# Performance work log

Hardware: AMD Instinct MI355X
Metric: run time of the kernel (lower is better)

Reference implementation:

```python
import jax, jax.numpy as jnp
import numpy as np

N = 4096
IN_DIM, HID, OUT_DIM = 512, 256, 64
PROP_STEP = 10
LAM_HAT = 0.9
SCAD_A = 3.7
EPS = 1e-8


def setup_inputs() -> dict:
    key = jax.random.key(0)
    kA, kF, k1, k2 = jax.random.split(key, 4)
    # sparse symmetric 0/1 adjacency, zero diagonal (add_loops adds I later)
    u = jax.random.uniform(kA, (N, N), dtype=jnp.float32)
    A = (u < 0.005).astype(jnp.float32)
    A = jnp.maximum(A, A.T)
    A = A * (1.0 - jnp.eye(N, dtype=jnp.float32))
    F = jax.random.normal(kF, (N, IN_DIM), dtype=jnp.float32)
    W1 = jax.random.normal(k1, (IN_DIM, HID), dtype=jnp.float32) / np.sqrt(IN_DIM)
    b1 = jnp.zeros((HID,), dtype=jnp.float32)
    W2 = jax.random.normal(k2, (HID, OUT_DIM), dtype=jnp.float32) / np.sqrt(HID)
    b2 = jnp.zeros((OUT_DIM,), dtype=jnp.float32)
    raw_gamma = jnp.zeros((PROP_STEP,), dtype=jnp.float32)
    return {"A": A, "F": F, "W1": W1, "b1": b1, "W2": W2, "b2": b2,
            "raw_gamma": raw_gamma}


def reference(A, F, W1, b1, W2, b2, raw_gamma):
    lam = 1.0 / LAM_HAT - 1.0
    a = SCAD_A
    # MLP (dropout inactive at inference)
    F0 = jax.nn.relu(F @ W1 + b1) @ W2 + b2            # [N, out_dim]
    eye = jnp.eye(A.shape[0], dtype=A.dtype)
    A = A + eye                                        # add_loops
    D = A.sum(-1)                                      # [N]
    D_sq = jnp.sqrt(D)[:, None]                        # [N, 1]
    A_tilde = A / D_sq / D_sq.T                        # sym_norm: D^-1/2 A D^-1/2
    gammas = jax.nn.sigmoid(raw_gamma) * 2.0           # per-layer gamma in (0, 2)

    def step(Fc, gamma_k):
        Fn = Fc / D_sq
        nrm = jnp.linalg.norm(Fn, axis=-1, keepdims=True)
        Fu = Fn / jnp.maximum(nrm, 1e-12)
        # cosine distance in [0, 2]; detached as in torch (.detach())
        y = jax.lax.stop_gradient(1.0 - Fu @ Fu.T)     # [N, N]
        lam_k = jnp.maximum(gamma_k / a, EPS)
        t = a * lam_k
        safe_y = jnp.where(y <= 0.0, 1.0, y)
        w_mid = (t - y) / ((a - 1.0) * safe_y)
        # SCAD weight: 1 for y<=lam_k, linear decay on [lam_k, a*lam_k], 0 beyond
        W = jnp.where(y <= lam_k, 1.0, jnp.where(y <= t, w_mid, 0.0))
        W = W * (1.0 - eye)
        W = jnp.where(jnp.isnan(W), 1.0, W)
        Q_hat = ((W * A).sum(-1) / D + lam)[:, None]   # [N, 1]
        F_new = (W * A_tilde) @ Fc / Q_hat + lam * F0 / Q_hat
        return F_new, None

    F_out, _ = jax.lax.scan(step, F0, gammas)
    return F_out
```

## Files before the change

kernel.cpp:

```cpp
#include <hip/hip_runtime.h>
#include <hip/hip_bf16.h>

#define N_NODES 4096
#define IN_DIM  512
#define HID_DIM 256
#define OUT_DIM 64
#define PROP_STEP 10
#define MAX_DEG 128
#define KSPLIT  4
#define LAM_CONST (1.0f/0.9f - 1.0f)
#define SCAD_A 3.7f

__device__ __forceinline__ ushort f2bf(float f) {
    unsigned u = __float_as_uint(f);
    unsigned r = (u + 0x7FFFu + ((u >> 16) & 1u)) >> 16;
    return (ushort)r;
}
__device__ __forceinline__ unsigned pack2(float lo, float hi) {
    return (unsigned)f2bf(lo) | ((unsigned)f2bf(hi) << 16);
}
__device__ __forceinline__ float bflo(unsigned u) { return __uint_as_float(u << 16); }
__device__ __forceinline__ float bfhi(unsigned u) { return __uint_as_float(u & 0xFFFF0000u); }

__device__ __forceinline__ float wave_reduce_add(float v) {
#pragma unroll
    for (int off = 32; off > 0; off >>= 1) v += __shfl_xor(v, off, 64);
    return v;
}

__global__ __launch_bounds__(256) void build_graph(
    const float* __restrict__ A, int* __restrict__ ell, int* __restrict__ deg,
    float* __restrict__ invD, float* __restrict__ invDsq)
{
    int i = blockIdx.x;
    int t = threadIdx.x;
    __shared__ int cnt;
    if (t == 0) cnt = 0;
    __syncthreads();
    const float4* row = (const float4*)(A + (size_t)i * N_NODES);
    for (int q = t; q < N_NODES / 4; q += 256) {
        float4 v = row[q];
        if (v.x != 0.0f) { int p = atomicAdd(&cnt, 1); if (p < MAX_DEG) ell[i * MAX_DEG + p] = q * 4 + 0; }
        if (v.y != 0.0f) { int p = atomicAdd(&cnt, 1); if (p < MAX_DEG) ell[i * MAX_DEG + p] = q * 4 + 1; }
        if (v.z != 0.0f) { int p = atomicAdd(&cnt, 1); if (p < MAX_DEG) ell[i * MAX_DEG + p] = q * 4 + 2; }
        if (v.w != 0.0f) { int p = atomicAdd(&cnt, 1); if (p < MAX_DEG) ell[i * MAX_DEG + p] = q * 4 + 3; }
    }
    __syncthreads();
    if (t == 0) {
        int c = cnt;
        if (c > MAX_DEG) c = MAX_DEG;
        deg[i] = c;
        int pad = (c + 15) & ~15;
        if (pad > MAX_DEG) pad = MAX_DEG;
        for (int p = c; p < pad; p++) ell[i * MAX_DEG + p] = i;
        float d = (float)(cnt + 1);
        invD[i] = 1.0f / d;
        invDsq[i] = rsqrtf(d);
    }
}

__global__ __launch_bounds__(256) void mlp1(
    const float* __restrict__ F, const float* __restrict__ W1,
    float* __restrict__ Hp)
{
    __shared__ float sA[16][68];
    __shared__ float sB[16][68];
    int t  = threadIdx.x;
    int m0 = blockIdx.x * 64;
    int n0 = blockIdx.y * 64;
    int kp = blockIdx.z;
    int tm = (t & 15) * 4;
    int tn = (t >> 4) * 4;
    int ar = t >> 2;
    int ac = (t & 3) * 4;
    int br = t >> 4;
    int bc = (t & 15) * 4;
    float acc[4][4] = {};
    int k0 = kp * (IN_DIM / KSPLIT);
    for (int kc = k0; kc < k0 + IN_DIM / KSPLIT; kc += 16) {
        float4 va = *(const float4*)(F  + (size_t)(m0 + ar) * IN_DIM + kc + ac);
        float4 vb = *(const float4*)(W1 + (size_t)(kc + br) * HID_DIM + n0 + bc);
        __syncthreads();
        sA[ac + 0][ar] = va.x;
        sA[ac + 1][ar] = va.y;
        sA[ac + 2][ar] = va.z;
        sA[ac + 3][ar] = va.w;
        *(float4*)&sB[br][bc] = vb;
        __syncthreads();
#pragma unroll
        for (int k = 0; k < 16; k++) {
            float4 a = *(const float4*)&sA[k][tm];
            float4 b = *(const float4*)&sB[k][tn];
            acc[0][0] += a.x * b.x; acc[0][1] += a.x * b.y; acc[0][2] += a.x * b.z; acc[0][3] += a.x * b.w;
            acc[1][0] += a.y * b.x; acc[1][1] += a.y * b.y; acc[1][2] += a.y * b.z; acc[1][3] += a.y * b.w;
            acc[2][0] += a.z * b.x; acc[2][1] += a.z * b.y; acc[2][2] += a.z * b.z; acc[2][3] += a.z * b.w;
            acc[3][0] += a.w * b.x; acc[3][1] += a.w * b.y; acc[3][2] += a.w * b.z; acc[3][3] += a.w * b.w;
        }
    }
    float* Hb = Hp + (size_t)kp * N_NODES * HID_DIM;
#pragma unroll
    for (int r = 0; r < 4; r++) {
        *(float4*)&Hb[(size_t)(m0 + tm + r) * HID_DIM + n0 + tn] =
            make_float4(acc[r][0], acc[r][1], acc[r][2], acc[r][3]);
    }
}

__global__ __launch_bounds__(256) void reduce_H(
    float* __restrict__ Hp, const float* __restrict__ b1)
{
    size_t idx = (size_t)blockIdx.x * 256 + threadIdx.x;
    const size_t PS = (size_t)N_NODES * HID_DIM / 4;
    float4* H4 = (float4*)Hp;
    float4 s0 = H4[idx], s1 = H4[idx + PS], s2 = H4[idx + 2 * PS], s3 = H4[idx + 3 * PS];
    int col4 = (int)((idx * 4) & (HID_DIM - 1));
    float4 bb = *(const float4*)(b1 + col4);
    float4 o;
    o.x = fmaxf(s0.x + s1.x + s2.x + s3.x + bb.x, 0.0f);
    o.y = fmaxf(s0.y + s1.y + s2.y + s3.y + bb.y, 0.0f);
    o.z = fmaxf(s0.z + s1.z + s2.z + s3.z + bb.z, 0.0f);
    o.w = fmaxf(s0.w + s1.w + s2.w + s3.w + bb.w, 0.0f);
    H4[idx] = o;
}

__global__ __launch_bounds__(256) void mlp2(
    const float* __restrict__ H, const float* __restrict__ W2,
    const float* __restrict__ b2, const float* __restrict__ invDsq,
    float* __restrict__ F0, unsigned* __restrict__ P0, float* __restrict__ nrm0)
{
    int wid = threadIdx.x >> 6, lane = threadIdx.x & 63;
    int row = blockIdx.x * 4 + wid;
    const float* h = H + (size_t)row * HID_DIM;
    float acc = b2[lane];
    for (int k = 0; k < HID_DIM; k += 4) {
        float4 hv = *(const float4*)(h + k);
        acc += hv.x * W2[(k + 0) * OUT_DIM + lane];
        acc += hv.y * W2[(k + 1) * OUT_DIM + lane];
        acc += hv.z * W2[(k + 2) * OUT_DIM + lane];
        acc += hv.w * W2[(k + 3) * OUT_DIM + lane];
    }
    size_t o = (size_t)row * OUT_DIM + lane;
    F0[o] = acc;
    float fn = acc * invDsq[row];
    float nrm = fmaxf(sqrtf(wave_reduce_add(fn * fn)), 1e-12f);
    float fu = fn / nrm;
    float fu_hi = __shfl_xor(fu, 1, 64);
    if ((lane & 1) == 0) {
        P0[(size_t)row * 32 + (lane >> 1)] = pack2(fu, fu_hi);
    }
    if (lane == 0) nrm0[row] = nrm;
}

__global__ __launch_bounds__(256, 8) void propagate(
    const unsigned* __restrict__ Pin, const float* __restrict__ nrmIn,
    const float* __restrict__ F0,
    const int* __restrict__ ell, const int* __restrict__ deg,
    const float* __restrict__ invD, const float* __restrict__ invDsq,
    const float* __restrict__ raw_gamma, int step,
    unsigned* __restrict__ Pout, float* __restrict__ nrmOut,
    float* __restrict__ FcOut, int writeNext, int writeOut)
{
    __shared__ float part[2][8][10];
    int lane = threadIdx.x & 63;
    int wid  = threadIdx.x >> 6;
    int h    = wid & 1;
    int rl   = wid >> 1;
    int r    = __builtin_amdgcn_readfirstlane(blockIdx.x * 2 + rl);
    int g    = lane >> 3;
    int sl   = lane & 7;
    const float inv_am1 = 1.0f / (SCAD_A - 1.0f);

    float gamma = 2.0f / (1.0f + expf(-raw_gamma[step]));
    float lam_k = fmaxf(gamma / SCAD_A, 1e-8f);
    float tt    = SCAD_A * lam_k;

    int dg = deg[r];
    int pad = (dg + 15) & ~15;
    int npair = pad >> 4;
    const int* nb = ell + (size_t)r * MAX_DEG;
    int ed0 = (lane < pad)      ? nb[lane]      : r;
    int ed1 = (64 + lane < pad) ? nb[64 + lane] : r;

    uint4 up = *(const uint4*)(Pin + (size_t)r * 32 + sl * 4);
    float ui[8] = { bflo(up.x), bfhi(up.x), bflo(up.y), bfhi(up.y),
                    bflo(up.z), bfhi(up.z), bflo(up.w), bfhi(up.w) };

    float acc[8] = {};
    float qsum = 0.0f;
    for (int it = h; it < npair; it += 2) {
        int e0 = it * 16 + g;
        int e1 = e0 + 8;
        int src = (it < 4) ? ed0 : ed1;
        int j0 = __shfl(src, e0 & 63, 64);
        int j1 = __shfl(src, e1 & 63, 64);
        uint4 u0 = *(const uint4*)(Pin + (size_t)j0 * 32 + sl * 4);
        uint4 u1 = *(const uint4*)(Pin + (size_t)j1 * 32 + sl * 4);
        float nr0 = nrmIn[j0];
        float nr1 = nrmIn[j1];

        float pa = ui[0] * bflo(u0.x) + ui[1] * bfhi(u0.x) + ui[2] * bflo(u0.y) + ui[3] * bfhi(u0.y)
                 + ui[4] * bflo(u0.z) + ui[5] * bfhi(u0.z) + ui[6] * bflo(u0.w) + ui[7] * bfhi(u0.w);
        float pb = ui[0] * bflo(u1.x) + ui[1] * bfhi(u1.x) + ui[2] * bflo(u1.y) + ui[3] * bfhi(u1.y)
                 + ui[4] * bflo(u1.z) + ui[5] * bfhi(u1.z) + ui[6] * bflo(u1.w) + ui[7] * bfhi(u1.w);
        pa += __shfl_xor(pa, 1, 64); pb += __shfl_xor(pb, 1, 64);
        pa += __shfl_xor(pa, 2, 64); pb += __shfl_xor(pb, 2, 64);
        pa += __shfl_xor(pa, 4, 64); pb += __shfl_xor(pb, 4, 64);
        float ya = 1.0f - pa, yb = 1.0f - pb;
        float wa = (ya <= lam_k) ? 1.0f : ((ya <= tt) ? (tt - ya) * inv_am1 / ya : 0.0f);
        float wb = (yb <= lam_k) ? 1.0f : ((yb <= tt) ? (tt - yb) * inv_am1 / yb : 0.0f);
        if (e0 >= dg) wa = 0.0f;
        if (e1 >= dg) wb = 0.0f;
        qsum += wa + wb;
        float wsa = wa * nr0;
        float wsb = wb * nr1;
        acc[0] += wsa * bflo(u0.x) + wsb * bflo(u1.x);
        acc[1] += wsa * bfhi(u0.x) + wsb * bfhi(u1.x);
        acc[2] += wsa * bflo(u0.y) + wsb * bflo(u1.y);
        acc[3] += wsa * bfhi(u0.y) + wsb * bfhi(u1.y);
        acc[4] += wsa * bflo(u0.z) + wsb * bflo(u1.z);
        acc[5] += wsa * bfhi(u0.z) + wsb * bfhi(u1.z);
        acc[6] += wsa * bflo(u0.w) + wsb * bflo(u1.w);
        acc[7] += wsa * bfhi(u0.w) + wsb * bfhi(u1.w);
    }

#pragma unroll
    for (int off = 8; off <= 32; off <<= 1) {
#pragma unroll
        for (int q = 0; q < 8; q++) acc[q] += __shfl_xor(acc[q], off, 64);
        qsum += __shfl_xor(qsum, off, 64);
    }

    if (h == 1 && lane < 8) {
#pragma unroll
        for (int q = 0; q < 8; q++) part[rl][sl][q] = acc[q];
        part[rl][sl][8] = qsum;
    }
    __syncthreads();
    if (h == 1) return;
    if (lane < 8) {
#pragma unroll
        for (int q = 0; q < 8; q++) acc[q] += part[rl][sl][q];
        qsum += part[rl][sl][8];
    }

    float iDs = invDsq[r];
    float Qh  = qsum * invD[r] + LAM_CONST;
    float rQh = 1.0f / Qh;
    const float4* f04 = (const float4*)(F0 + (size_t)r * OUT_DIM + sl * 8);
    float4 f0a = f04[0], f0b = f04[1];
    float f0v[8] = { f0a.x, f0a.y, f0a.z, f0a.w, f0b.x, f0b.y, f0b.z, f0b.w };
    float res[8];
#pragma unroll
    for (int q = 0; q < 8; q++) res[q] = (acc[q] * iDs + LAM_CONST * f0v[q]) * rQh;

    if (writeOut && lane < 8) {
        float4* o4 = (float4*)(FcOut + (size_t)r * OUT_DIM + sl * 8);
        o4[0] = make_float4(res[0], res[1], res[2], res[3]);
        o4[1] = make_float4(res[4], res[5], res[6], res[7]);
    }
    if (writeNext) {
        float fn[8];
        float ssq = 0.0f;
#pragma unroll
        for (int q = 0; q < 8; q++) { fn[q] = res[q] * iDs; ssq += fn[q] * fn[q]; }
        ssq += __shfl_xor(ssq, 1, 64);
        ssq += __shfl_xor(ssq, 2, 64);
        ssq += __shfl_xor(ssq, 4, 64);
        float nrm = fmaxf(sqrtf(ssq), 1e-12f);
        float inv_n = 1.0f / nrm;
        if (lane < 8) {
            uint4 fuPk;
            fuPk.x = pack2(fn[0] * inv_n, fn[1] * inv_n);
            fuPk.y = pack2(fn[2] * inv_n, fn[3] * inv_n);
            fuPk.z = pack2(fn[4] * inv_n, fn[5] * inv_n);
            fuPk.w = pack2(fn[6] * inv_n, fn[7] * inv_n);
            *(uint4*)(Pout + (size_t)r * 32 + sl * 4) = fuPk;
        }
        if (lane == 0) nrmOut[r] = nrm;
    }
}

extern "C" void kernel_launch(void* const* d_in, const int* in_sizes, int n_in,
                              void* d_out, int out_size, void* d_ws, size_t ws_size,
                              hipStream_t stream)
{
    const float* A  = (const float*)d_in[0];
    const float* F  = (const float*)d_in[1];
    const float* W1 = (const float*)d_in[2];
    const float* b1 = (const float*)d_in[3];
    const float* W2 = (const float*)d_in[4];
    const float* b2 = (const float*)d_in[5];
    const float* rg = (const float*)d_in[6];
    float* out = (float*)d_out;

    char* p = (char*)d_ws;
    float* Hp     = (float*)p; p += (size_t)KSPLIT * N_NODES * HID_DIM * 4;
    float* F0     = (float*)p; p += (size_t)N_NODES * OUT_DIM * 4;
    unsigned* Pa  = (unsigned*)p; p += (size_t)N_NODES * 32 * 4;
    unsigned* Pb  = (unsigned*)p; p += (size_t)N_NODES * 32 * 4;
    float* nrmA   = (float*)p; p += (size_t)N_NODES * 4;
    float* nrmB   = (float*)p; p += (size_t)N_NODES * 4;
    float* invD   = (float*)p; p += (size_t)N_NODES * 4;
    float* invDsq = (float*)p; p += (size_t)N_NODES * 4;
    int*   deg    = (int*)p;   p += (size_t)N_NODES * 4;
    int*   ell    = (int*)p;   p += (size_t)N_NODES * MAX_DEG * 4;

    build_graph<<<N_NODES, 256, 0, stream>>>(A, ell, deg, invD, invDsq);
    mlp1<<<dim3(N_NODES / 64, HID_DIM / 64, KSPLIT), 256, 0, stream>>>(F, W1, Hp);
    reduce_H<<<N_NODES * HID_DIM / 4 / 256, 256, 0, stream>>>(Hp, b1);
    mlp2<<<N_NODES / 4, 256, 0, stream>>>(Hp, W2, b2, invDsq, F0, Pa, nrmA);

    for (int k = 0; k < PROP_STEP; k++) {
        unsigned* Pin   = (k & 1) ? Pb : Pa;
        unsigned* Pout  = (k & 1) ? Pa : Pb;
        float* nIn      = (k & 1) ? nrmB : nrmA;
        float* nOut     = (k & 1) ? nrmA : nrmB;
        int last = (k == PROP_STEP - 1);
        propagate<<<N_NODES / 2, 256, 0, stream>>>(
            Pin, nIn, F0, ell, deg, invD, invDsq, rg, k,
            Pout, nOut, out, !last, last);
    }
}
```

Measured before the change: 231.4 us.

## Merge graph build with MLP1 and fuse split-K reduce into MLP2

Runs the graph-building blocks and the first MLP GEMM blocks in a single launch, so the two independent phases can overlap and one launch is saved. The split-K reduction, bias and ReLU are folded into the second MLP kernel, which also stages W2 and the hidden row in shared memory. This removes two kernel launches and one full round trip of the hidden activations through global memory. In exchange, each mlp2 block now copies all of W2 (64 KB) into shared memory, which lowers occupancy and repeats that load across 1024 blocks.

```diff
diff --git a/kernel.cpp b/kernel.cpp
--- a/kernel.cpp
+++ b/kernel.cpp
@@ -8,6 +8,7 @@
 #define PROP_STEP 10
 #define MAX_DEG 128
 #define KSPLIT  4
+#define MLP1_BLOCKS (64 * 4 * KSPLIT)
 #define LAM_CONST (1.0f/0.9f - 1.0f)
 #define SCAD_A 3.7f
 
@@ -28,116 +29,122 @@
     return v;
 }
 
-__global__ __launch_bounds__(256) void build_graph(
-    const float* __restrict__ A, int* __restrict__ ell, int* __restrict__ deg,
+__global__ __launch_bounds__(256) void build_mlp1(
+    const float* __restrict__ A, const float* __restrict__ F,
+    const float* __restrict__ W1, float* __restrict__ Hp,
+    int* __restrict__ ell, int* __restrict__ deg,
     float* __restrict__ invD, float* __restrict__ invDsq)
 {
-    int i = blockIdx.x;
-    int t = threadIdx.x;
-    __shared__ int cnt;
-    if (t == 0) cnt = 0;
-    __syncthreads();
-    const float4* row = (const float4*)(A + (size_t)i * N_NODES);
-    for (int q = t; q < N_NODES / 4; q += 256) {
-        float4 v = row[q];
-        if (v.x != 0.0f) { int p = atomicAdd(&cnt, 1); if (p < MAX_DEG) ell[i * MAX_DEG + p] = q * 4 + 0; }
-        if (v.y != 0.0f) { int p = atomicAdd(&cnt, 1); if (p < MAX_DEG) ell[i * MAX_DEG + p] = q * 4 + 1; }
-        if (v.z != 0.0f) { int p = atomicAdd(&cnt, 1); if (p < MAX_DEG) ell[i * MAX_DEG + p] = q * 4 + 2; }
-        if (v.w != 0.0f) { int p = atomicAdd(&cnt, 1); if (p < MAX_DEG) ell[i * MAX_DEG + p] = q * 4 + 3; }
-    }
-    __syncthreads();
-    if (t == 0) {
-        int c = cnt;
-        if (c > MAX_DEG) c = MAX_DEG;
-        deg[i] = c;
-        int pad = (c + 15) & ~15;
-        if (pad > MAX_DEG) pad = MAX_DEG;
-        for (int p = c; p < pad; p++) ell[i * MAX_DEG + p] = i;
-        float d = (float)(cnt + 1);
-        invD[i] = 1.0f / d;
-        invDsq[i] = rsqrtf(d);
-    }
-}
-
-__global__ __launch_bounds__(256) void mlp1(
-    const float* __restrict__ F, const float* __restrict__ W1,
-    float* __restrict__ Hp)
-{
-    __shared__ float sA[16][68];
-    __shared__ float sB[16][68];
-    int t  = threadIdx.x;
-    int m0 = blockIdx.x * 64;
-    int n0 = blockIdx.y * 64;
-    int kp = blockIdx.z;
-    int tm = (t & 15) * 4;
-    int tn = (t >> 4) * 4;
-    int ar = t >> 2;
-    int ac = (t & 3) * 4;
-    int br = t >> 4;
-    int bc = (t & 15) * 4;
-    float acc[4][4] = {};
-    int k0 = kp * (IN_DIM / KSPLIT);
-    for (int kc = k0; kc < k0 + IN_DIM / KSPLIT; kc += 16) {
-        float4 va = *(const float4*)(F  + (size_t)(m0 + ar) * IN_DIM + kc + ac);
-        float4 vb = *(const float4*)(W1 + (size_t)(kc + br) * HID_DIM + n0 + bc);
+    if (blockIdx.x < MLP1_BLOCKS) {
+        __shared__ float sA[16][68];
+        __shared__ float sB[16][68];
+        int bid = blockIdx.x;
+        int t  = threadIdx.x;
+        int m0 = (bid & 63) * 64;
+        int n0 = ((bid >> 6) & 3) * 64;
+        int kp = bid >> 8;
+        int tm = (t & 15) * 4;
+        int tn = (t >> 4) * 4;
+        int ar = t >> 2;
+        int ac = (t & 3) * 4;
+        int br = t >> 4;
+        int bc = (t & 15) * 4;
+        float acc[4][4] = {};
+        int k0 = kp * (IN_DIM / KSPLIT);
+        for (int kc = k0; kc < k0 + IN_DIM / KSPLIT; kc += 16) {
+            float4 va = *(const float4*)(F  + (size_t)(m0 + ar) * IN_DIM + kc + ac);
+            float4 vb = *(const float4*)(W1 + (size_t)(kc + br) * HID_DIM + n0 + bc);
+            __syncthreads();
+            sA[ac + 0][ar] = va.x;
+            sA[ac + 1][ar] = va.y;
+            sA[ac + 2][ar] = va.z;
+            sA[ac + 3][ar] = va.w;
+            *(float4*)&sB[br][bc] = vb;
+            __syncthreads();
+#pragma unroll
+            for (int k = 0; k < 16; k++) {
+                float4 a = *(const float4*)&sA[k][tm];
+                float4 b = *(const float4*)&sB[k][tn];
+                acc[0][0] += a.x * b.x; acc[0][1] += a.x * b.y; acc[0][2] += a.x * b.z; acc[0][3] += a.x * b.w;
+                acc[1][0] += a.y * b.x; acc[1][1] += a.y * b.y; acc[1][2] += a.y * b.z; acc[1][3] += a.y * b.w;
+                acc[2][0] += a.z * b.x; acc[2][1] += a.z * b.y; acc[2][2] += a.z * b.z; acc[2][3] += a.z * b.w;
+                acc[3][0] += a.w * b.x; acc[3][1] += a.w * b.y; acc[3][2] += a.w * b.z; acc[3][3] += a.w * b.w;
+            }
+        }
+        float* Hb = Hp + (size_t)kp * N_NODES * HID_DIM;
+#pragma unroll
+        for (int r = 0; r < 4; r++) {
+            *(float4*)&Hb[(size_t)(m0 + tm + r) * HID_DIM + n0 + tn] =
+                make_float4(acc[r][0], acc[r][1], acc[r][2], acc[r][3]);
+        }
+    } else {
+        __shared__ int cnt;
+        int i = blockIdx.x - MLP1_BLOCKS;
+        int t = threadIdx.x;
+        if (t == 0) cnt = 0;
         __syncthreads();
-        sA[ac + 0][ar] = va.x;
-        sA[ac + 1][ar] = va.y;
-        sA[ac + 2][ar] = va.z;
-        sA[ac + 3][ar] = va.w;
-        *(float4*)&sB[br][bc] = vb;
+        const float4* row = (const float4*)(A + (size_t)i * N_NODES);
+        for (int q = t; q < N_NODES / 4; q += 256) {
+            float4 v = row[q];
+            if (v.x != 0.0f) { int p = atomicAdd(&cnt, 1); if (p < MAX_DEG) ell[i * MAX_DEG + p] = q * 4 + 0; }
+            if (v.y != 0.0f) { int p = atomicAdd(&cnt, 1); if (p < MAX_DEG) ell[i * MAX_DEG + p] = q * 4 + 1; }
+            if (v.z != 0.0f) { int p = atomicAdd(&cnt, 1); if (p < MAX_DEG) ell[i * MAX_DEG + p] = q * 4 + 2; }
+            if (v.w != 0.0f) { int p = atomicAdd(&cnt, 1); if (p < MAX_DEG) ell[i * MAX_DEG + p] = q * 4 + 3; }
+        }
         __syncthreads();
-#pragma unroll
-        for (int k = 0; k < 16; k++) {
-            float4 a = *(const float4*)&sA[k][tm];
-            float4 b = *(const float4*)&sB[k][tn];
-            acc[0][0] += a.x * b.x; acc[0][1] += a.x * b.y; acc[0][2] += a.x * b.z; acc[0][3] += a.x * b.w;
-            acc[1][0] += a.y * b.x; acc[1][1] += a.y * b.y; acc[1][2] += a.y * b.z; acc[1][3] += a.y * b.w;
-            acc[2][0] += a.z * b.x; acc[2][1] += a.z * b.y; acc[2][2] += a.z * b.z; acc[2][3] += a.z * b.w;
-            acc[3][0] += a.w * b.x; acc[3][1] += a.w * b.y; acc[3][2] += a.w * b.z; acc[3][3] += a.w * b.w;
-        }
-    }
-    float* Hb = Hp + (size_t)kp * N_NODES * HID_DIM;
-#pragma unroll
-    for (int r = 0; r < 4; r++) {
-        *(float4*)&Hb[(size_t)(m0 + tm + r) * HID_DIM + n0 + tn] =
-            make_float4(acc[r][0], acc[r][1], acc[r][2], acc[r][3]);
-    }
-}
-
-__global__ __launch_bounds__(256) void reduce_H(
-    float* __restrict__ Hp, const float* __restrict__ b1)
-{
-    size_t idx = (size_t)blockIdx.x * 256 + threadIdx.x;
-    const size_t PS = (size_t)N_NODES * HID_DIM / 4;
-    float4* H4 = (float4*)Hp;
-    float4 s0 = H4[idx], s1 = H4[idx + PS], s2 = H4[idx + 2 * PS], s3 = H4[idx + 3 * PS];
-    int col4 = (int)((idx * 4) & (HID_DIM - 1));
-    float4 bb = *(const float4*)(b1 + col4);
-    float4 o;
-    o.x = fmaxf(s0.x + s1.x + s2.x + s3.x + bb.x, 0.0f);
-    o.y = fmaxf(s0.y + s1.y + s2.y + s3.y + bb.y, 0.0f);
-    o.z = fmaxf(s0.z + s1.z + s2.z + s3.z + bb.z, 0.0f);
-    o.w = fmaxf(s0.w + s1.w + s2.w + s3.w + bb.w, 0.0f);
-    H4[idx] = o;
-}
-
-__global__ __launch_bounds__(256) void mlp2(
-    const float* __restrict__ H, const float* __restrict__ W2,
-    const float* __restrict__ b2, const float* __restrict__ invDsq,
+        if (t == 0) {
+            int c = cnt;
+            if (c > MAX_DEG) c = MAX_DEG;
+            deg[i] = c;
+            int pad = (c + 15) & ~15;
+            if (pad > MAX_DEG) pad = MAX_DEG;
+            for (int p = c; p < pad; p++) ell[i * MAX_DEG + p] = i;
+            float d = (float)(cnt + 1);
+            invD[i] = 1.0f / d;
+            invDsq[i] = rsqrtf(d);
+        }
+    }
+}
+
+__global__ __launch_bounds__(256) void mlp2r(
+    const float* __restrict__ Hp, const float* __restrict__ b1,
+    const float* __restrict__ W2, const float* __restrict__ b2,
+    const float* __restrict__ invDsq,
     float* __restrict__ F0, unsigned* __restrict__ P0, float* __restrict__ nrm0)
 {
-    int wid = threadIdx.x >> 6, lane = threadIdx.x & 63;
-    int row = blockIdx.x * 4 + wid;
-    const float* h = H + (size_t)row * HID_DIM;
+    __shared__ float sW2[HID_DIM * OUT_DIM];
+    __shared__ float hbuf[4][HID_DIM];
+    int tid  = threadIdx.x;
+    int wid  = tid >> 6, lane = tid & 63;
+    int row  = blockIdx.x * 4 + wid;
+    const size_t PS = (size_t)N_NODES * HID_DIM;
+
+    for (int i = tid; i < HID_DIM * OUT_DIM / 4; i += 256)
+        ((float4*)sW2)[i] = ((const float4*)W2)[i];
+
+    const float* hrow = Hp + (size_t)row * HID_DIM + lane * 4;
+    float4 s0 = *(const float4*)(hrow);
+    float4 s1 = *(const float4*)(hrow + PS);
+    float4 s2 = *(const float4*)(hrow + 2 * PS);
+    float4 s3 = *(const float4*)(hrow + 3 * PS);
+    float4 bb = *(const float4*)(b1 + lane * 4);
+    float h0 = fmaxf(s0.x + s1.x + s2.x + s3.x + bb.x, 0.0f);
+    float h1 = fmaxf(s0.y + s1.y + s2.y + s3.y + bb.y, 0.0f);
+    float h2 = fmaxf(s0.z + s1.z + s2.z + s3.z + bb.z, 0.0f);
+    float h3 = fmaxf(s0.w + s1.w + s2.w + s3.w + bb.w, 0.0f);
+    __syncthreads();
+    hbuf[wid][lane * 4 + 0] = h0;
+    hbuf[wid][lane * 4 + 1] = h1;
+    hbuf[wid][lane * 4 + 2] = h2;
+    hbuf[wid][lane * 4 + 3] = h3;
+    __syncthreads();
+
     float acc = b2[lane];
-    for (int k = 0; k < HID_DIM; k += 4) {
-        float4 hv = *(const float4*)(h + k);
-        acc += hv.x * W2[(k + 0) * OUT_DIM + lane];
-        acc += hv.y * W2[(k + 1) * OUT_DIM + lane];
-        acc += hv.z * W2[(k + 2) * OUT_DIM + lane];
-        acc += hv.w * W2[(k + 3) * OUT_DIM + lane];
-    }
+#pragma unroll 8
+    for (int k = 0; k < HID_DIM; k++) {
+        acc += hbuf[wid][k] * sW2[k * OUT_DIM + lane];
+    }
+
     size_t o = (size_t)row * OUT_DIM + lane;
     F0[o] = acc;
     float fn = acc * invDsq[row];
@@ -304,10 +311,9 @@
     int*   deg    = (int*)p;   p += (size_t)N_NODES * 4;
     int*   ell    = (int*)p;   p += (size_t)N_NODES * MAX_DEG * 4;
 
-    build_graph<<<N_NODES, 256, 0, stream>>>(A, ell, deg, invD, invDsq);
-    mlp1<<<dim3(N_NODES / 64, HID_DIM / 64, KSPLIT), 256, 0, stream>>>(F, W1, Hp);
-    reduce_H<<<N_NODES * HID_DIM / 4 / 256, 256, 0, stream>>>(Hp, b1);
-    mlp2<<<N_NODES / 4, 256, 0, stream>>>(Hp, W2, b2, invDsq, F0, Pa, nrmA);
+    build_mlp1<<<MLP1_BLOCKS + N_NODES, 256, 0, stream>>>(
+        A, F, W1, Hp, ell, deg, invD, invDsq);
+    mlp2r<<<N_NODES / 4, 256, 0, stream>>>(Hp, b1, W2, b2, invDsq, F0, Pa, nrmA);
 
     for (int k = 0; k < PROP_STEP; k++) {
         unsigned* Pin   = (k & 1) ? Pb : Pa;
```

After: 226.9 us. About the same (-2.0%).
